# Kernel tuning notes

Measured on AMD Instinct MI355X. Metric: run time of the kernel, lower is better.

The kernel has to match this reference:

```python
import jax, jax.numpy as jnp
import numpy as np
import math

B, S, E, H = 2, 2048, 1024, 16
HD = E // H          # head_dim = 64
HX = 64              # helix_dim
P = HX // 2          # helix pairs = 32

def setup_inputs() -> dict:
    key = jax.random.key(0)
    ks = jax.random.split(key, 12)
    sc = 0.02
    return {
        "x":    jax.random.normal(ks[0], (B, S, E), dtype=jnp.float32),
        "Wq":   jax.random.normal(ks[1], (E, E), dtype=jnp.float32) * sc,
        "bq":   jnp.zeros((E,), dtype=jnp.float32),
        "Wk":   jax.random.normal(ks[2], (E, E), dtype=jnp.float32) * sc,
        "bk":   jnp.zeros((E,), dtype=jnp.float32),
        "Wv":   jax.random.normal(ks[3], (E, E), dtype=jnp.float32) * sc,
        "bv":   jnp.zeros((E,), dtype=jnp.float32),
        "Wo":   jax.random.normal(ks[4], (E, E), dtype=jnp.float32) * sc,
        "bo":   jnp.zeros((E,), dtype=jnp.float32),
        "Whel": jax.random.normal(ks[5], (H, HX, HD), dtype=jnp.float32) * sc,
        "bhel": jnp.zeros((H, HX), dtype=jnp.float32),
    }

def _l2norm(x, eps=1e-12):
    # torch F.normalize(p=2, dim=-1): x / max(||x||, eps)
    n = jnp.sqrt(jnp.sum(x * x, axis=-1, keepdims=True))
    return x / jnp.maximum(n, eps)

def _scramble(t):
    # faithful to torch: (B,S,2) -> transpose(1,2) -> reshape(B,S,2),
    # vectorized over (H,P): t is (B,H,P,S,2)
    b, h, p, s, _ = t.shape
    return jnp.swapaxes(t, -1, -2).reshape(b, h, p, s, 2)

def reference(x, Wq, bq, Wk, bk, Wv, bv, Wo, bo, Whel, bhel):
    b, s, e = x.shape
    h, hx, hd = Whel.shape
    p = hx // 2
    q = x @ Wq.T + bq
    k = x @ Wk.T + bk
    v = x @ Wv.T + bv
    qh = q.reshape(b, s, h, hd)
    kh = k.reshape(b, s, h, hd)
    # per-head helical projections: (B,S,H,HX)
    q_hel = jnp.einsum('bshd,hed->bshe', qh, Whel) + bhel
    k_hel = jnp.einsum('bshd,hed->bshe', kh, Whel) + bhel
    # split into 2D coords, normalize each pair: (B,H,P,S,2)
    qn = _l2norm(q_hel.reshape(b, s, h, p, 2)).transpose(0, 2, 3, 1, 4)
    kn = _l2norm(k_hel.reshape(b, s, h, p, 2)).transpose(0, 2, 3, 1, 4)
    qn = _scramble(qn)
    kn = _scramble(kn)
    # helical similarity averaged over pairs: (B,H,S,S)
    helical = jnp.einsum('bhpsc,bhptc->bhst', qn, kn) / p
    # standard scaled dot-product scores
    dot = jnp.einsum('bshd,bthd->bhst', qh, kh) / math.sqrt(hd)
    alpha = 0.5
    attn = jax.nn.softmax(alpha * dot + (1.0 - alpha) * helical, axis=-1)
    vh = v.reshape(b, s, h, hd)
    out = jnp.einsum('bhst,bthd->bshd', attn, vh).reshape(b, s, e)
    return out @ Wo.T + bo
```

## Files before the change

kernel.cpp:

```cpp
#include <hip/hip_runtime.h>
#include <hip/hip_bf16.h>


typedef unsigned short u16;
typedef unsigned int u32;
typedef __attribute__((ext_vector_type(8))) __bf16 bf16x8;
typedef __attribute__((ext_vector_type(4))) float f32x4;

__device__ __forceinline__ u16 f2b(float f) {
  u32 u = __float_as_uint(f);
  u32 r = (u + 0x7fffu + ((u >> 16) & 1u)) >> 16;
  return (u16)r;
}
__device__ __forceinline__ float b2f(u16 h) {
  return __uint_as_float(((u32)h) << 16);
}

__device__ __forceinline__ f32x4 mfma16(bf16x8 a, bf16x8 b, f32x4 c) {
  return __builtin_amdgcn_mfma_f32_16x16x32_bf16(a, b, c, 0, 0, 0);
}

__device__ __forceinline__ void gld16(void* lds, const void* g) {
  __builtin_amdgcn_global_load_lds(
      (const __attribute__((address_space(1))) unsigned int*)g,
      (__attribute__((address_space(3))) unsigned int*)lds, 16, 0, 0);
}

__global__ __launch_bounds__(256) void cast_kernel(
    const float* __restrict__ x,  const float* __restrict__ wq,
    const float* __restrict__ wk, const float* __restrict__ wv,
    const float* __restrict__ wo, const float* __restrict__ whel,
    u16* __restrict__ xb, u16* __restrict__ wb, u16* __restrict__ wob,
    u16* __restrict__ whb) {
  long long q = (long long)blockIdx.x * 256 + threadIdx.x;
  const float* s; u16* d; long long base;
  if (q < 1048576)      { s = x;    d = xb;            base = 0; }
  else if (q < 1310720) { s = wq;   d = wb;            base = 1048576; }
  else if (q < 1572864) { s = wk;   d = wb + 1048576;  base = 1310720; }
  else if (q < 1835008) { s = wv;   d = wb + 2097152;  base = 1572864; }
  else if (q < 2097152) { s = wo;   d = wob;           base = 1835008; }
  else                  { s = whel; d = whb;           base = 2097152; }
  long long e = (q - base) * 4;
  float4 v = *(const float4*)(s + e);
  ushort4 o;
  o.x = f2b(v.x); o.y = f2b(v.y); o.z = f2b(v.z); o.w = f2b(v.w);
  *(ushort4*)(d + e) = o;
}

__global__ __launch_bounds__(256, 2) void qkv_gemm(
    const u16* __restrict__ xb, const u16* __restrict__ wb,
    const float* __restrict__ bq, const float* __restrict__ bk,
    const float* __restrict__ bv,
    u16* __restrict__ Qcat, u16* __restrict__ Kcat, u16* __restrict__ vt) {
  __shared__ u16 Al[128][32];
  __shared__ u16 Bl[128][32];
  const int nt = blockIdx.x, mt = blockIdx.y;
  const int which = nt >> 3;
  const int n0 = (nt & 7) << 7;
  const int m0 = mt << 7;
  const int tid = threadIdx.x;
  const int wave = tid >> 6, lane = tid & 63;
  const int g = lane >> 4, c15 = lane & 15;
  const int wm = wave & 1, wn = wave >> 1;
  const u16* Wp = wb + (long long)which * (1024 * 1024) + n0 * 1024;
  const u16* Ap = xb + m0 * 1024;
  const int srow = (wave * 64 + lane) >> 2;
  const int scol = (lane & 3) << 3;

  f32x4 acc[4][4];
#pragma unroll
  for (int i = 0; i < 4; i++)
#pragma unroll
    for (int j = 0; j < 4; j++) acc[i][j] = f32x4{0.f, 0.f, 0.f, 0.f};

  for (int k0 = 0; k0 < 1024; k0 += 32) {
    gld16(&Al[srow][scol],      Ap + srow * 1024 + k0 + scol);
    gld16(&Al[64 + srow][scol], Ap + (64 + srow) * 1024 + k0 + scol);
    gld16(&Bl[srow][scol],      Wp + srow * 1024 + k0 + scol);
    gld16(&Bl[64 + srow][scol], Wp + (64 + srow) * 1024 + k0 + scol);
    __syncthreads();
    bf16x8 a[4], b[4];
#pragma unroll
    for (int i = 0; i < 4; i++)
      a[i] = *(const bf16x8*)&Al[wm * 64 + i * 16 + c15][g * 8];
#pragma unroll
    for (int j = 0; j < 4; j++)
      b[j] = *(const bf16x8*)&Bl[wn * 64 + j * 16 + c15][g * 8];
#pragma unroll
    for (int i = 0; i < 4; i++)
#pragma unroll
      for (int j = 0; j < 4; j++) acc[i][j] = mfma16(a[i], b[j], acc[i][j]);
    __syncthreads();
  }

  const float* bias = (which == 0) ? bq : ((which == 1) ? bk : bv);
#pragma unroll
  for (int i = 0; i < 4; i++)
#pragma unroll
    for (int j = 0; j < 4; j++)
#pragma unroll
      for (int r = 0; r < 4; r++) {
        int row = m0 + wm * 64 + i * 16 + g * 4 + r;
        int col = n0 + wn * 64 + j * 16 + c15;
        float v = acc[i][j][r] + bias[col];
        int bb = row >> 11, s = row & 2047;
        int hh = col >> 6, d = col & 63;
        if (which == 0) {
          Qcat[(((bb * 16 + hh) * 2048) + s) * 128 + d] = f2b(v * 0.0625f);
        } else if (which == 1) {
          Kcat[(((bb * 16 + hh) * 2048) + s) * 128 + d] = f2b(v);
        } else {
          vt[((bb * 16 + hh) * 64 + d) * 2048 + s] = f2b(v);
        }
      }
}

__global__ __launch_bounds__(256, 2) void helical_kernel(
    u16* __restrict__ Qcat, u16* __restrict__ Kcat,
    const u16* __restrict__ whb, const float* __restrict__ bhel) {
  __shared__ u16 A[2][2][64][32];
  __shared__ u16 Wl[2][64][32];
  const int sb = blockIdx.x, bh = blockIdx.y;
  const int h = bh & 15;
  const int s0 = sb << 6;
  const int tid = threadIdx.x;
  const int wave = tid >> 6, lane = tid & 63;
  const int g = lane >> 4, c15 = lane & 15;
  u16* Qb = Qcat + (long long)bh * (2048 * 128);
  u16* Kb = Kcat + (long long)bh * (2048 * 128);

#pragma unroll
  for (int it = 0; it < 2; ++it) {
    int cidx = it * 256 + tid;
    int e = cidx >> 3, ds = (cidx & 7) << 3;
    uint4 vv = *(const uint4*)(whb + h * 4096 + e * 64 + ds);
    *(uint4*)&Wl[ds >> 5][e][ds & 31] = vv;
  }
#pragma unroll
  for (int it = 0; it < 4; ++it) {
    int cidx = it * 256 + tid;
    int which = cidx >> 9;
    int r = (cidx >> 3) & 63;
    int ds = (cidx & 7) << 3;
    const u16* src = (which ? Kb : Qb) + (s0 + r) * 128 + ds;
    uint4 vv = *(const uint4*)src;
    if (which == 0) {
      u16 tmp[8];
      *(uint4*)tmp = vv;
#pragma unroll
      for (int q = 0; q < 8; ++q) tmp[q] = f2b(b2f(tmp[q]) * 16.0f);
      vv = *(uint4*)tmp;
    }
    *(uint4*)&A[which][ds >> 5][r][ds & 31] = vv;
  }
  __syncthreads();

  const int which = wave >> 1, hf = wave & 1;
  f32x4 acc[2][4];
#pragma unroll
  for (int i = 0; i < 2; i++)
#pragma unroll
    for (int j = 0; j < 4; j++) acc[i][j] = f32x4{0.f, 0.f, 0.f, 0.f};
#pragma unroll
  for (int kq = 0; kq < 2; ++kq) {
    bf16x8 a0 = *(const bf16x8*)&A[which][kq][hf * 32 + c15][g * 8];
    bf16x8 a1 = *(const bf16x8*)&A[which][kq][hf * 32 + 16 + c15][g * 8];
#pragma unroll
    for (int j = 0; j < 4; ++j) {
      bf16x8 bb = *(const bf16x8*)&Wl[kq][j * 16 + c15][g * 8];
      acc[0][j] = mfma16(a0, bb, acc[0][j]);
      acc[1][j] = mfma16(a1, bb, acc[1][j]);
    }
  }
  u16* Dst = which ? Kb : Qb;
#pragma unroll
  for (int i = 0; i < 2; ++i)
#pragma unroll
    for (int j = 0; j < 4; ++j)
#pragma unroll
      for (int r = 0; r < 4; ++r) {
        int s_loc = hf * 32 + i * 16 + g * 4 + r;
        int e = j * 16 + c15;
        float v = acc[i][j][r] + bhel[h * 64 + e];
        float pp = __shfl_xor(v, 1);
        float nn = sqrtf(v * v + pp * pp);
        float o = v / fmaxf(nn, 1e-12f) * 0.125f;
        int s = s0 + s_loc;
        int u = s >> 1, c2 = s & 1;
        int row_out = ((e & 1) ? 1024 : 0) + u;
        int col_out = 64 + (e & ~1) + c2;
        Dst[row_out * 128 + col_out] = f2b(o);
      }
}

__global__ __launch_bounds__(256, 2) void attn_kernel(
    const u16* __restrict__ Qcat, const u16* __restrict__ Kcat,
    const u16* __restrict__ vt, u16* __restrict__ AO) {
  __shared__ u16 Kl[4][64][32];
  __shared__ u16 Vl[2][64][32];
  __shared__ u16 Pl[2][128][32];
  const int qt = blockIdx.x, bh = blockIdx.y;
  const int bb = bh >> 4, h = bh & 15;
  const int q0 = qt << 7;
  const int tid = threadIdx.x;
  const int wave = tid >> 6, lane = tid & 63;
  const int g = lane >> 4, c15 = lane & 15;
  const u16* Qb = Qcat + (long long)bh * (2048 * 128);
  const u16* Kb = Kcat + (long long)bh * (2048 * 128);
  const u16* Vb = vt + (long long)bh * (64 * 2048);
  const int r4 = (wave * 64 + lane) >> 2;
  const int c8 = (lane & 3) << 3;
  const int lin8 = (wave * 64 + lane) * 8;

  bf16x8 qf[2][4];
#pragma unroll
  for (int i = 0; i < 2; ++i)
#pragma unroll
    for (int kq = 0; kq < 4; ++kq)
      qf[i][kq] = *(const bf16x8*)(Qb + (q0 + wave * 32 + i * 16 + c15) * 128 +
                                   kq * 32 + g * 8);

  f32x4 accO[2][4];
  float den[2][4];
#pragma unroll
  for (int i = 0; i < 2; i++)
#pragma unroll
    for (int j = 0; j < 4; j++) accO[i][j] = f32x4{0.f, 0.f, 0.f, 0.f};
#pragma unroll
  for (int i = 0; i < 2; i++)
#pragma unroll
    for (int r = 0; r < 4; r++) den[i][r] = 0.f;

  for (int t = 0; t < 32; ++t) {
    const int t0 = t << 6;
#pragma unroll
    for (int kq = 0; kq < 4; ++kq)
      gld16(((u16*)Kl) + kq * 2048 + lin8, Kb + (t0 + r4) * 128 + kq * 32 + c8);
#pragma unroll
    for (int tq = 0; tq < 2; ++tq)
      gld16(((u16*)Vl) + tq * 2048 + lin8, Vb + r4 * 2048 + t0 + tq * 32 + c8);
    __syncthreads();

    f32x4 accS[2][4];
#pragma unroll
    for (int i = 0; i < 2; i++)
#pragma unroll
      for (int j = 0; j < 4; j++) accS[i][j] = f32x4{0.f, 0.f, 0.f, 0.f};
#pragma unroll
    for (int kq = 0; kq < 4; ++kq) {
#pragma unroll
      for (int j = 0; j < 4; ++j) {
        bf16x8 bk2 = *(const bf16x8*)&Kl[kq][j * 16 + c15][g * 8];
        accS[0][j] = mfma16(qf[0][kq], bk2, accS[0][j]);
        accS[1][j] = mfma16(qf[1][kq], bk2, accS[1][j]);
      }
    }

#pragma unroll
    for (int i = 0; i < 2; ++i) {
      float rs[4] = {0.f, 0.f, 0.f, 0.f};
#pragma unroll
      for (int j = 0; j < 4; ++j) {
        int tq = j >> 1;
        int tc = ((j & 1) << 4) + c15;
        int mrow = wave * 32 + i * 16 + g * 4;
#pragma unroll
        for (int r = 0; r < 4; ++r) {
          float p = __expf(accS[i][j][r]);
          rs[r] += p;
          Pl[tq][mrow + r][tc] = f2b(p);
        }
      }
#pragma unroll
      for (int r = 0; r < 4; ++r) {
        float v = rs[r];
        v += __shfl_xor(v, 1);
        v += __shfl_xor(v, 2);
        v += __shfl_xor(v, 4);
        v += __shfl_xor(v, 8);
        den[i][r] += v;
      }
    }

#pragma unroll
    for (int tq = 0; tq < 2; ++tq) {
      bf16x8 a0 = *(const bf16x8*)&Pl[tq][wave * 32 + c15][g * 8];
      bf16x8 a1 = *(const bf16x8*)&Pl[tq][wave * 32 + 16 + c15][g * 8];
#pragma unroll
      for (int j = 0; j < 4; ++j) {
        bf16x8 bv2 = *(const bf16x8*)&Vl[tq][j * 16 + c15][g * 8];
        accO[0][j] = mfma16(a0, bv2, accO[0][j]);
        accO[1][j] = mfma16(a1, bv2, accO[1][j]);
      }
    }
    __syncthreads();
  }

#pragma unroll
  for (int i = 0; i < 2; ++i)
#pragma unroll
    for (int j = 0; j < 4; ++j)
#pragma unroll
      for (int r = 0; r < 4; ++r) {
        int m = wave * 32 + i * 16 + g * 4 + r;
        int s = q0 + m;
        float o = accO[i][j][r] / den[i][r];
        int d = j * 16 + c15;
        AO[((bb * 2048 + s) * 1024) + h * 64 + d] = f2b(o);
      }
}

__global__ __launch_bounds__(256, 2) void out_gemm(
    const u16* __restrict__ AO, const u16* __restrict__ wob,
    const float* __restrict__ bo, float* __restrict__ out) {
  __shared__ u16 Al[128][32];
  __shared__ u16 Bl[128][32];
  const int n0 = blockIdx.x << 7;
  const int m0 = blockIdx.y << 7;
  const int tid = threadIdx.x;
  const int wave = tid >> 6, lane = tid & 63;
  const int g = lane >> 4, c15 = lane & 15;
  const int wm = wave & 1, wn = wave >> 1;
  const u16* Wp = wob + n0 * 1024;
  const u16* Ap = AO + m0 * 1024;
  const int srow = (wave * 64 + lane) >> 2;
  const int scol = (lane & 3) << 3;

  f32x4 acc[4][4];
#pragma unroll
  for (int i = 0; i < 4; i++)
#pragma unroll
    for (int j = 0; j < 4; j++) acc[i][j] = f32x4{0.f, 0.f, 0.f, 0.f};

  for (int k0 = 0; k0 < 1024; k0 += 32) {
    gld16(&Al[srow][scol],      Ap + srow * 1024 + k0 + scol);
    gld16(&Al[64 + srow][scol], Ap + (64 + srow) * 1024 + k0 + scol);
    gld16(&Bl[srow][scol],      Wp + srow * 1024 + k0 + scol);
    gld16(&Bl[64 + srow][scol], Wp + (64 + srow) * 1024 + k0 + scol);
    __syncthreads();
    bf16x8 a[4], b[4];
#pragma unroll
    for (int i = 0; i < 4; i++)
      a[i] = *(const bf16x8*)&Al[wm * 64 + i * 16 + c15][g * 8];
#pragma unroll
    for (int j = 0; j < 4; j++)
      b[j] = *(const bf16x8*)&Bl[wn * 64 + j * 16 + c15][g * 8];
#pragma unroll
    for (int i = 0; i < 4; i++)
#pragma unroll
      for (int j = 0; j < 4; j++) acc[i][j] = mfma16(a[i], b[j], acc[i][j]);
    __syncthreads();
  }
#pragma unroll
  for (int i = 0; i < 4; i++)
#pragma unroll
    for (int j = 0; j < 4; j++)
#pragma unroll
      for (int r = 0; r < 4; r++) {
        int row = m0 + wm * 64 + i * 16 + g * 4 + r;
        int col = n0 + wn * 64 + j * 16 + c15;
        out[row * 1024 + col] = acc[i][j][r] + bo[col];
      }
}

extern "C" void kernel_launch(void* const* d_in, const int* in_sizes, int n_in,
                              void* d_out, int out_size, void* d_ws,
                              size_t ws_size, hipStream_t stream) {
  const float* x    = (const float*)d_in[0];
  const float* Wq   = (const float*)d_in[1];
  const float* bq   = (const float*)d_in[2];
  const float* Wk   = (const float*)d_in[3];
  const float* bk   = (const float*)d_in[4];
  const float* Wv   = (const float*)d_in[5];
  const float* bv   = (const float*)d_in[6];
  const float* Wo   = (const float*)d_in[7];
  const float* bo   = (const float*)d_in[8];
  const float* Whel = (const float*)d_in[9];
  const float* bhel = (const float*)d_in[10];
  float* out = (float*)d_out;

  char* ws = (char*)d_ws;
  u16* xb   = (u16*)(ws + 0);
  u16* wb   = (u16*)(ws + 8388608);
  u16* wob  = (u16*)(ws + 14680064);
  u16* whb  = (u16*)(ws + 16777216);
  u16* Qcat = (u16*)(ws + 16908288);
  u16* Kcat = (u16*)(ws + 33685504);
  u16* vt   = (u16*)(ws + 50462720);
  u16* AO   = (u16*)(ws + 58851328);

  dim3 blk(256);
  cast_kernel<<<dim3(8256), blk, 0, stream>>>(x, Wq, Wk, Wv, Wo, Whel, xb, wb,
                                              wob, whb);
  qkv_gemm<<<dim3(24, 32), blk, 0, stream>>>(xb, wb, bq, bk, bv, Qcat, Kcat,
                                             vt);
  helical_kernel<<<dim3(32, 32), blk, 0, stream>>>(Qcat, Kcat, whb, bhel);
  attn_kernel<<<dim3(16, 32), blk, 0, stream>>>(Qcat, Kcat, vt, AO);
  out_gemm<<<dim3(8, 32), blk, 0, stream>>>(AO, wob, bo, out);
}
```

Before: 270.1 us.

## Shrink attention query tile to 64 rows and transpose V via LDS in QKV GEMM

The attention kernel now handles 64 query rows per block instead of 128, one 16-row tile per wave, and launches twice as many blocks with a higher occupancy hint. It also pads the P buffer in LDS, moves the row-sum shuffle reduction out of the loop to the end, and rounds P to bf16 by truncation. Separately, the QKV GEMM writes transposed V through an LDS staging tile so the global stores are coalesced 16-byte writes rather than scattered 2-byte stores. The trade-off is more K/V reloads per query row and slightly less accurate P rounding.

```diff
diff --git a/kernel.cpp b/kernel.cpp
--- a/kernel.cpp
+++ b/kernel.cpp
@@ -54,6 +54,7 @@
     u16* __restrict__ Qcat, u16* __restrict__ Kcat, u16* __restrict__ vt) {
   __shared__ u16 Al[128][32];
   __shared__ u16 Bl[128][32];
+  __shared__ u16 T[64][136];
   const int nt = blockIdx.x, mt = blockIdx.y;
   const int which = nt >> 3;
   const int n0 = (nt & 7) << 7;
@@ -93,7 +94,41 @@
     __syncthreads();
   }
 
-  const float* bias = (which == 0) ? bq : ((which == 1) ? bk : bv);
+  if (which == 2) {
+#pragma unroll
+    for (int half = 0; half < 2; ++half) {
+      __syncthreads();
+      if (wn == half) {
+#pragma unroll
+        for (int i = 0; i < 4; i++)
+#pragma unroll
+          for (int j = 0; j < 4; j++)
+#pragma unroll
+            for (int r = 0; r < 4; r++) {
+              int nloc = j * 16 + c15;
+              int mloc = wm * 64 + i * 16 + g * 4 + r;
+              float v = acc[i][j][r] + bv[n0 + half * 64 + nloc];
+              T[nloc][mloc] = f2b(v);
+            }
+      }
+      __syncthreads();
+#pragma unroll
+      for (int it = 0; it < 4; ++it) {
+        int idx = it * 256 + tid;
+        int row = idx >> 4;
+        int cm = (idx & 15) * 8;
+        int col = n0 + half * 64 + row;
+        int hh = col >> 6, dd = col & 63;
+        int m = m0 + cm;
+        int bb2 = m >> 11, s = m & 2047;
+        *(uint4*)&vt[(((bb2 * 16 + hh) * 64) + dd) * 2048 + s] =
+            *(const uint4*)&T[row][cm];
+      }
+    }
+    return;
+  }
+
+  const float* bias = (which == 0) ? bq : bk;
 #pragma unroll
   for (int i = 0; i < 4; i++)
 #pragma unroll
@@ -107,10 +142,8 @@
         int hh = col >> 6, d = col & 63;
         if (which == 0) {
           Qcat[(((bb * 16 + hh) * 2048) + s) * 128 + d] = f2b(v * 0.0625f);
-        } else if (which == 1) {
+        } else {
           Kcat[(((bb * 16 + hh) * 2048) + s) * 128 + d] = f2b(v);
-        } else {
-          vt[((bb * 16 + hh) * 64 + d) * 2048 + s] = f2b(v);
         }
       }
 }
@@ -193,15 +226,15 @@
       }
 }
 
-__global__ __launch_bounds__(256, 2) void attn_kernel(
+__global__ __launch_bounds__(256, 4) void attn_kernel(
     const u16* __restrict__ Qcat, const u16* __restrict__ Kcat,
     const u16* __restrict__ vt, u16* __restrict__ AO) {
   __shared__ u16 Kl[4][64][32];
   __shared__ u16 Vl[2][64][32];
-  __shared__ u16 Pl[2][128][32];
+  __shared__ u16 Pl[2][64][40];
   const int qt = blockIdx.x, bh = blockIdx.y;
   const int bb = bh >> 4, h = bh & 15;
-  const int q0 = qt << 7;
+  const int q0 = qt << 6;
   const int tid = threadIdx.x;
   const int wave = tid >> 6, lane = tid & 63;
   const int g = lane >> 4, c15 = lane & 15;
@@ -212,24 +245,18 @@
   const int c8 = (lane & 3) << 3;
   const int lin8 = (wave * 64 + lane) * 8;
 
-  bf16x8 qf[2][4];
-#pragma unroll
-  for (int i = 0; i < 2; ++i)
-#pragma unroll
-    for (int kq = 0; kq < 4; ++kq)
-      qf[i][kq] = *(const bf16x8*)(Qb + (q0 + wave * 32 + i * 16 + c15) * 128 +
-                                   kq * 32 + g * 8);
-
-  f32x4 accO[2][4];
-  float den[2][4];
-#pragma unroll
-  for (int i = 0; i < 2; i++)
-#pragma unroll
-    for (int j = 0; j < 4; j++) accO[i][j] = f32x4{0.f, 0.f, 0.f, 0.f};
-#pragma unroll
-  for (int i = 0; i < 2; i++)
-#pragma unroll
-    for (int r = 0; r < 4; r++) den[i][r] = 0.f;
+  bf16x8 qf[4];
+#pragma unroll
+  for (int kq = 0; kq < 4; ++kq)
+    qf[kq] = *(const bf16x8*)(Qb + (q0 + wave * 16 + c15) * 128 + kq * 32 +
+                              g * 8);
+
+  f32x4 accO[4];
+  float den[4];
+#pragma unroll
+  for (int j = 0; j < 4; j++) accO[j] = f32x4{0.f, 0.f, 0.f, 0.f};
+#pragma unroll
+  for (int r = 0; r < 4; r++) den[r] = 0.f;
 
   for (int t = 0; t < 32; ++t) {
     const int t0 = t << 6;
@@ -241,73 +268,62 @@
       gld16(((u16*)Vl) + tq * 2048 + lin8, Vb + r4 * 2048 + t0 + tq * 32 + c8);
     __syncthreads();
 
-    f32x4 accS[2][4];
-#pragma unroll
-    for (int i = 0; i < 2; i++)
-#pragma unroll
-      for (int j = 0; j < 4; j++) accS[i][j] = f32x4{0.f, 0.f, 0.f, 0.f};
+    f32x4 accS[4];
+#pragma unroll
+    for (int j = 0; j < 4; j++) accS[j] = f32x4{0.f, 0.f, 0.f, 0.f};
 #pragma unroll
     for (int kq = 0; kq < 4; ++kq) {
 #pragma unroll
       for (int j = 0; j < 4; ++j) {
         bf16x8 bk2 = *(const bf16x8*)&Kl[kq][j * 16 + c15][g * 8];
-        accS[0][j] = mfma16(qf[0][kq], bk2, accS[0][j]);
-        accS[1][j] = mfma16(qf[1][kq], bk2, accS[1][j]);
-      }
-    }
-
-#pragma unroll
-    for (int i = 0; i < 2; ++i) {
-      float rs[4] = {0.f, 0.f, 0.f, 0.f};
-#pragma unroll
-      for (int j = 0; j < 4; ++j) {
-        int tq = j >> 1;
-        int tc = ((j & 1) << 4) + c15;
-        int mrow = wave * 32 + i * 16 + g * 4;
-#pragma unroll
-        for (int r = 0; r < 4; ++r) {
-          float p = __expf(accS[i][j][r]);
-          rs[r] += p;
-          Pl[tq][mrow + r][tc] = f2b(p);
-        }
-      }
+        accS[j] = mfma16(qf[kq], bk2, accS[j]);
+      }
+    }
+
+#pragma unroll
+    for (int j = 0; j < 4; ++j) {
+      int tq = j >> 1;
+      int tc = ((j & 1) << 4) + c15;
+      int mrow = wave * 16 + g * 4;
 #pragma unroll
       for (int r = 0; r < 4; ++r) {
-        float v = rs[r];
-        v += __shfl_xor(v, 1);
-        v += __shfl_xor(v, 2);
-        v += __shfl_xor(v, 4);
-        v += __shfl_xor(v, 8);
-        den[i][r] += v;
+        float p = __expf(accS[j][r]);
+        den[r] += p;
+        Pl[tq][mrow + r][tc] = (u16)(__float_as_uint(p) >> 16);
       }
     }
 
 #pragma unroll
     for (int tq = 0; tq < 2; ++tq) {
-      bf16x8 a0 = *(const bf16x8*)&Pl[tq][wave * 32 + c15][g * 8];
-      bf16x8 a1 = *(const bf16x8*)&Pl[tq][wave * 32 + 16 + c15][g * 8];
+      bf16x8 a = *(const bf16x8*)&Pl[tq][wave * 16 + c15][g * 8];
 #pragma unroll
       for (int j = 0; j < 4; ++j) {
         bf16x8 bv2 = *(const bf16x8*)&Vl[tq][j * 16 + c15][g * 8];
-        accO[0][j] = mfma16(a0, bv2, accO[0][j]);
-        accO[1][j] = mfma16(a1, bv2, accO[1][j]);
-      }
-    }
-    __syncthreads();
-  }
-
-#pragma unroll
-  for (int i = 0; i < 2; ++i)
-#pragma unroll
-    for (int j = 0; j < 4; ++j)
-#pragma unroll
-      for (int r = 0; r < 4; ++r) {
-        int m = wave * 32 + i * 16 + g * 4 + r;
-        int s = q0 + m;
-        float o = accO[i][j][r] / den[i][r];
-        int d = j * 16 + c15;
-        AO[((bb * 2048 + s) * 1024) + h * 64 + d] = f2b(o);
-      }
+        accO[j] = mfma16(a, bv2, accO[j]);
+      }
+    }
+    __syncthreads();
+  }
+
+#pragma unroll
+  for (int r = 0; r < 4; ++r) {
+    float v = den[r];
+    v += __shfl_xor(v, 1);
+    v += __shfl_xor(v, 2);
+    v += __shfl_xor(v, 4);
+    v += __shfl_xor(v, 8);
+    den[r] = v;
+  }
+
+#pragma unroll
+  for (int j = 0; j < 4; ++j)
+#pragma unroll
+    for (int r = 0; r < 4; ++r) {
+      int s = q0 + wave * 16 + g * 4 + r;
+      float o = accO[j][r] / den[r];
+      int d = j * 16 + c15;
+      AO[((bb * 2048 + s) * 1024) + h * 64 + d] = f2b(o);
+    }
 }
 
 __global__ __launch_bounds__(256, 2) void out_gemm(
@@ -395,6 +411,6 @@
   qkv_gemm<<<dim3(24, 32), blk, 0, stream>>>(xb, wb, bq, bk, bv, Qcat, Kcat,
                                              vt);
   helical_kernel<<<dim3(32, 32), blk, 0, stream>>>(Qcat, Kcat, whb, bhel);
-  attn_kernel<<<dim3(16, 32), blk, 0, stream>>>(Qcat, Kcat, vt, AO);
+  attn_kernel<<<dim3(32, 32), blk, 0, stream>>>(Qcat, Kcat, vt, AO);
   out_gemm<<<dim3(8, 32), blk, 0, stream>>>(AO, wob, bo, out);
 }
```

Result: faster. 254.6 us (-5.7%).
